# Kernel tuning notes

Measured on AMD Instinct MI355X. Metric: run time of the kernel, lower is better.

## Reference

```python
import jax, jax.numpy as jnp
import numpy as np
from jax import lax

GROUPS = 32
EPS = 1e-5
COMMON_STRIDE = 4


def conv3x3(x, w):
    # x: [B,C,H,W], w: [O,I,3,3], stride 1, padding 1 ('SAME'), no bias
    return lax.conv_general_dilated(x, w, (1, 1), 'SAME',
                                    dimension_numbers=('NCHW', 'OIHW', 'NCHW'))


def group_norm(x, scale, bias):
    b, c, h, w = x.shape
    xg = x.reshape(b, GROUPS, c // GROUPS, h, w)
    mean = xg.mean(axis=(2, 3, 4), keepdims=True)
    var = xg.var(axis=(2, 3, 4), keepdims=True)
    xg = (xg - mean) * lax.rsqrt(var + EPS)
    x = xg.reshape(b, c, h, w)
    return x * scale[None, :, None, None] + bias[None, :, None, None]


def head(x, w, s, bta):
    return jax.nn.relu(group_norm(conv3x3(x, w), s, bta))


def setup_inputs() -> dict:
    key = jax.random.key(0)
    ks = jax.random.split(key, 4)
    B, Cin, H, W = 2, 256, 64, 64
    Cd, K = 128, 19
    fan3 = Cin * 9
    return {
        'x': jax.random.normal(ks[0], (B, Cin, H, W), jnp.float32),
        'w_pam': jax.random.normal(ks[1], (Cd, Cin, 3, 3), jnp.float32) * np.sqrt(2.0 / fan3),
        'gn_pam_scale': jnp.ones((Cd,), jnp.float32),
        'gn_pam_bias': jnp.zeros((Cd,), jnp.float32),
        'w_cam': jax.random.normal(ks[2], (Cd, Cin, 3, 3), jnp.float32) * np.sqrt(2.0 / fan3),
        'gn_cam_scale': jnp.ones((Cd,), jnp.float32),
        'gn_cam_bias': jnp.zeros((Cd,), jnp.float32),
        'w_pred': jax.random.normal(ks[3], (K, Cd, 1, 1), jnp.float32) * np.sqrt(2.0 / Cd),
        'b_pred': jnp.zeros((K,), jnp.float32),
    }


def reference(x, w_pam, gn_pam_scale, gn_pam_bias, w_cam, gn_cam_scale, gn_cam_bias,
              w_pred, b_pred):
    pam = head(x, w_pam, gn_pam_scale, gn_pam_bias)   # [B,C,H,W]
    cam = head(x, w_cam, gn_cam_scale, gn_cam_bias)   # [B,C,H,W]
    b, c, h, w = pam.shape
    n = h * w

    # --- PAM: spatial self-attention, unscaled QK^T softmax V (Q=K=V=pam) ---
    Bm = pam.reshape(b, c, n)                                   # [B,C,N]
    pam_w = jax.nn.softmax(jnp.einsum('bci,bcj->bij', Bm, Bm), axis=-1)  # [B,N,N]
    weighted_pam = jnp.einsum('bij,bcj->bci', pam_w, Bm).reshape(b, c, h, w)
    sum_pam = pam + weighted_pam

    # --- CAM: channel self-attention over [C,C] gram matrix ---
    Am = cam.reshape(b, c, n)                                   # [B,C,N]
    cam_w = jax.nn.softmax(jnp.einsum('bcn,bdn->bcd', Am, Am), axis=-1)  # [B,C,C]
    weighted_cam = jnp.einsum('bcd,bdn->bcn', cam_w, Am).reshape(b, c, h, w)
    sum_cam = cam + weighted_cam

    # --- predictor (1x1 conv with bias) + bilinear upsample x common_stride ---
    fused = sum_pam + sum_cam
    logits = jnp.einsum('bchw,kc->bkhw', fused, w_pred[:, :, 0, 0]) + b_pred[None, :, None, None]
    out = jax.image.resize(logits, (b, logits.shape[1], h * COMMON_STRIDE, w * COMMON_STRIDE),
                           method='bilinear')  # half-pixel centers == align_corners=False
    return out
```

## Files before the change

kernel.cpp:

```cpp
#include <hip/hip_runtime.h>

#define BB 2
#define CIN 256
#define HH 64
#define WW 64
#define NPIX 4096
#define CD 128
#define CO2 256
#define KOUT 19
#define EPSV 1e-5f
#define SPAD 4356
#define KW9 2304

typedef __attribute__((ext_vector_type(8))) short bf16x8;
typedef __attribute__((ext_vector_type(4))) float f32x4;

__device__ inline unsigned short f2bf(float f) {
  unsigned u = __float_as_uint(f);
  u += 0x7fffu + ((u >> 16) & 1u);
  return (unsigned short)(u >> 16);
}
__device__ inline float bf2f(unsigned short h) {
  return __uint_as_float((unsigned)h << 16);
}
__device__ inline void f2bf_pair(float f, unsigned short& hi, unsigned short& lo) {
  hi = f2bf(f);
  const float fhi = __uint_as_float((unsigned)hi << 16);
  lo = f2bf(f - fhi);
}

__global__ __launch_bounds__(256) void zfill_kernel(uint4* __restrict__ p)
{
  const int i = blockIdx.x * 256 + threadIdx.x;
  if (i < 557568) p[i] = make_uint4(0, 0, 0, 0);
}

__global__ __launch_bounds__(256) void xpose_kernel(
    const float* __restrict__ x, unsigned short* __restrict__ xThi,
    unsigned short* __restrict__ xTlo)
{
  const int y = blockIdx.x;
  const int cig = blockIdx.y;
  const int b = blockIdx.z;
  __shared__ float Tl[32][65];
  const int t = threadIdx.x;
  {
    const int cl = t >> 3, pg = t & 7;
    const float* src = x + ((size_t)(b * CIN + cig * 32 + cl)) * NPIX + y * 64 + pg * 8;
    const float4 v0 = *reinterpret_cast<const float4*>(src);
    const float4 v1 = *reinterpret_cast<const float4*>(src + 4);
    Tl[cl][pg * 8 + 0] = v0.x; Tl[cl][pg * 8 + 1] = v0.y;
    Tl[cl][pg * 8 + 2] = v0.z; Tl[cl][pg * 8 + 3] = v0.w;
    Tl[cl][pg * 8 + 4] = v1.x; Tl[cl][pg * 8 + 5] = v1.y;
    Tl[cl][pg * 8 + 6] = v1.z; Tl[cl][pg * 8 + 7] = v1.w;
  }
  __syncthreads();
  {
    const int sl = t >> 2, cg = t & 3;
    unsigned short hh[8], ll[8];
    #pragma unroll
    for (int i = 0; i < 8; ++i) f2bf_pair(Tl[cg * 8 + i][sl], hh[i], ll[i]);
    uint4 ph, pl;
    ph.x = (unsigned)hh[0] | ((unsigned)hh[1] << 16);
    ph.y = (unsigned)hh[2] | ((unsigned)hh[3] << 16);
    ph.z = (unsigned)hh[4] | ((unsigned)hh[5] << 16);
    ph.w = (unsigned)hh[6] | ((unsigned)hh[7] << 16);
    pl.x = (unsigned)ll[0] | ((unsigned)ll[1] << 16);
    pl.y = (unsigned)ll[2] | ((unsigned)ll[3] << 16);
    pl.z = (unsigned)ll[4] | ((unsigned)ll[5] << 16);
    pl.w = (unsigned)ll[6] | ((unsigned)ll[7] << 16);
    const size_t o = ((size_t)b * SPAD + (y + 1) * 66 + 1 + sl) * 256 + cig * 32 + cg * 8;
    *reinterpret_cast<uint4*>(&xThi[o]) = ph;
    *reinterpret_cast<uint4*>(&xTlo[o]) = pl;
  }
}

__global__ __launch_bounds__(256) void wbconv_kernel(
    const float* __restrict__ w_pam, const float* __restrict__ w_cam,
    unsigned short* __restrict__ wbhi, unsigned short* __restrict__ wblo)
{
  const int co = blockIdx.x;
  const float* wsrc = (co < CD) ? (w_pam + (size_t)co * KW9)
                                : (w_cam + (size_t)(co - CD) * KW9);
  const int t = threadIdx.x;
  #pragma unroll
  for (int i = 0; i < 9; ++i) {
    const int idx = i * 256 + t;
    const int q = idx >> 8, ci = idx & 255;
    unsigned short h, l;
    f2bf_pair(wsrc[ci * 9 + q], h, l);
    const size_t dest = ((((size_t)(co >> 4) * 9 + q) * 8 + (ci >> 5)) * 4
                        + ((ci >> 3) & 3)) * 128 + (co & 15) * 8 + (ci & 7);
    wbhi[dest] = h;
    wblo[dest] = l;
  }
}

__global__ __launch_bounds__(256) void conv_mfma_kernel(
    const unsigned short* __restrict__ xThi, const unsigned short* __restrict__ xTlo,
    const unsigned short* __restrict__ wbhi, const unsigned short* __restrict__ wblo,
    float* __restrict__ out)
{
  const int pxt = blockIdx.x;
  const int cot = blockIdx.y;
  const int b = blockIdx.z;
  const int tid = threadIdx.x;
  const int w = tid >> 6;
  const int lane = tid & 63;
  const int m = lane & 15, g = lane >> 4;
  const int p0 = pxt * 64;
  const int y = p0 >> 6;
  const int sbase = (y + 1) * 66 + 1;

  __shared__ float Obuf[4][64][68];

  const size_t xb = (size_t)b * SPAD * 256;

  f32x4 acc[4][4];
  #pragma unroll
  for (int mt = 0; mt < 4; ++mt)
    #pragma unroll
    for (int jg = 0; jg < 4; ++jg)
      #pragma unroll
      for (int r = 0; r < 4; ++r) acc[mt][jg][r] = 0.f;

  for (int q = 0; q < 9; ++q) {
    const int dq = (q / 3 - 1) * 66 + (q % 3 - 1);
    const unsigned short* xh0 = xThi + xb + (size_t)(sbase + m + dq) * 256;
    const unsigned short* xl0 = xTlo + xb + (size_t)(sbase + m + dq) * 256;
    #pragma unroll
    for (int kk2 = 0; kk2 < 2; ++kk2) {
      const int kkc = w * 2 + kk2;
      const int ko = kkc * 32 + g * 8;
      bf16x8 bh[4], bl[4];
      #pragma unroll
      for (int jg = 0; jg < 4; ++jg) {
        bh[jg] = *reinterpret_cast<const bf16x8*>(&xh0[(size_t)(jg * 16) * 256 + ko]);
        bl[jg] = *reinterpret_cast<const bf16x8*>(&xl0[(size_t)(jg * 16) * 256 + ko]);
      }
      #pragma unroll
      for (int mt = 0; mt < 4; ++mt) {
        const size_t wbase = ((((size_t)(cot * 4 + mt) * 9 + q) * 8 + kkc) * 4 + g) * 128
                             + m * 8;
        const bf16x8 ah = *reinterpret_cast<const bf16x8*>(&wbhi[wbase]);
        const bf16x8 al = *reinterpret_cast<const bf16x8*>(&wblo[wbase]);
        #pragma unroll
        for (int jg = 0; jg < 4; ++jg) {
          acc[mt][jg] = __builtin_amdgcn_mfma_f32_16x16x32_bf16(ah, bh[jg], acc[mt][jg], 0, 0, 0);
          acc[mt][jg] = __builtin_amdgcn_mfma_f32_16x16x32_bf16(ah, bl[jg], acc[mt][jg], 0, 0, 0);
          acc[mt][jg] = __builtin_amdgcn_mfma_f32_16x16x32_bf16(al, bh[jg], acc[mt][jg], 0, 0, 0);
        }
      }
    }
  }

  #pragma unroll
  for (int mt = 0; mt < 4; ++mt)
    #pragma unroll
    for (int jg = 0; jg < 4; ++jg)
      #pragma unroll
      for (int r = 0; r < 4; ++r)
        Obuf[w][mt * 16 + g * 4 + r][jg * 16 + m] = acc[mt][jg][r];
  __syncthreads();

  const int co_l = tid >> 2;
  const int pxq = (tid & 3) * 16;
  float* op = out + ((size_t)b * CO2 + cot * 64 + co_l) * NPIX + p0 + pxq;
  #pragma unroll
  for (int i = 0; i < 4; ++i) {
    float4 s;
    s.x = Obuf[0][co_l][pxq + i * 4 + 0] + Obuf[1][co_l][pxq + i * 4 + 0]
        + Obuf[2][co_l][pxq + i * 4 + 0] + Obuf[3][co_l][pxq + i * 4 + 0];
    s.y = Obuf[0][co_l][pxq + i * 4 + 1] + Obuf[1][co_l][pxq + i * 4 + 1]
        + Obuf[2][co_l][pxq + i * 4 + 1] + Obuf[3][co_l][pxq + i * 4 + 1];
    s.z = Obuf[0][co_l][pxq + i * 4 + 2] + Obuf[1][co_l][pxq + i * 4 + 2]
        + Obuf[2][co_l][pxq + i * 4 + 2] + Obuf[3][co_l][pxq + i * 4 + 2];
    s.w = Obuf[0][co_l][pxq + i * 4 + 3] + Obuf[1][co_l][pxq + i * 4 + 3]
        + Obuf[2][co_l][pxq + i * 4 + 3] + Obuf[3][co_l][pxq + i * 4 + 3];
    *reinterpret_cast<float4*>(&op[i * 4]) = s;
  }
}

__global__ __launch_bounds__(256) void gn_stats_kernel(
    const float* __restrict__ conv, float* __restrict__ meanb, float* __restrict__ rstdb)
{
  const int g = blockIdx.x;
  const float* base = conv + (size_t)g * (4 * NPIX);
  float s = 0.f, ss = 0.f;
  const float4* b4 = reinterpret_cast<const float4*>(base);
  for (int i = threadIdx.x; i < 4096; i += 256) {
    float4 v = b4[i];
    s += v.x + v.y + v.z + v.w;
    ss += v.x * v.x + v.y * v.y + v.z * v.z + v.w * v.w;
  }
  #pragma unroll
  for (int off = 32; off > 0; off >>= 1) {
    s += __shfl_down(s, off);
    ss += __shfl_down(ss, off);
  }
  __shared__ float rs[4], rss[4];
  const int lane = threadIdx.x & 63, wv = threadIdx.x >> 6;
  if (lane == 0) { rs[wv] = s; rss[wv] = ss; }
  __syncthreads();
  if (threadIdx.x == 0) {
    const float S = rs[0] + rs[1] + rs[2] + rs[3];
    const float SS = rss[0] + rss[1] + rss[2] + rss[3];
    const float inv = 1.f / 16384.f;
    const float m = S * inv;
    const float var = SS * inv - m * m;
    meanb[g] = m;
    rstdb[g] = rsqrtf(var + EPSV);
  }
}

__global__ __launch_bounds__(256) void gn_apply_kernel(
    float* __restrict__ conv, const float* __restrict__ meanb, const float* __restrict__ rstdb,
    const float* __restrict__ sc_pam, const float* __restrict__ bi_pam,
    const float* __restrict__ sc_cam, const float* __restrict__ bi_cam)
{
  const int idx = blockIdx.x * 256 + threadIdx.x;
  const int call = (idx >> 12) & 255;
  const int g = idx >> 14;
  const int head = call >> 7;
  const int c = call & 127;
  const float sc = head ? sc_cam[c] : sc_pam[c];
  const float bi = head ? bi_cam[c] : bi_pam[c];
  const float v = conv[idx];
  const float r = (v - meanb[g]) * rstdb[g] * sc + bi;
  conv[idx] = fmaxf(r, 0.f);
}

__global__ __launch_bounds__(256) void pack_kv_kernel(
    const float* __restrict__ conv, unsigned short* __restrict__ Kf2,
    unsigned short* __restrict__ Vf2)
{
  const int px0 = blockIdx.x * 64;
  const int c0  = blockIdx.y * 32;
  const int b   = blockIdx.z;
  __shared__ unsigned short Tl[32][76];
  const int t = threadIdx.x;
  {
    const int cl = t >> 3, pg = t & 7;
    const float* src = conv + ((size_t)b * CO2 + c0 + cl) * NPIX + px0 + pg * 8;
    const float4 v0 = *reinterpret_cast<const float4*>(src);
    const float4 v1 = *reinterpret_cast<const float4*>(src + 4);
    Tl[cl][pg * 8 + 0] = f2bf(v0.x); Tl[cl][pg * 8 + 1] = f2bf(v0.y);
    Tl[cl][pg * 8 + 2] = f2bf(v0.z); Tl[cl][pg * 8 + 3] = f2bf(v0.w);
    Tl[cl][pg * 8 + 4] = f2bf(v1.x); Tl[cl][pg * 8 + 5] = f2bf(v1.y);
    Tl[cl][pg * 8 + 6] = f2bf(v1.z); Tl[cl][pg * 8 + 7] = f2bf(v1.w);
  }
  __syncthreads();
  unsigned short* Kb = Kf2 + (size_t)b * 524288;
  unsigned short* Vb = Vf2 + (size_t)b * 524288;
  {
    const int jblk_l = t >> 6, rem = t & 63;
    const int gk = rem >> 4, mk = rem & 15;
    const int jblk = (px0 >> 4) + jblk_l;
    const int kk = c0 >> 5;
    unsigned short h[8];
    #pragma unroll
    for (int e = 0; e < 8; ++e) h[e] = Tl[gk * 8 + e][jblk_l * 16 + mk];
    uint4 packed;
    packed.x = (unsigned)h[0] | ((unsigned)h[1] << 16);
    packed.y = (unsigned)h[2] | ((unsigned)h[3] << 16);
    packed.z = (unsigned)h[4] | ((unsigned)h[5] << 16);
    packed.w = (unsigned)h[6] | ((unsigned)h[7] << 16);
    *reinterpret_cast<uint4*>(&Kb[(size_t)(jblk * 16 + kk * 4 + gk) * 128 + mk * 8]) = packed;
  }
  {
    const int ct_l = t >> 7, kt = (t >> 6) & 1, gv = (t >> 4) & 3, mv = t & 15;
    const int ct = (c0 >> 4) + ct_l;
    const int jc = px0 >> 6;
    unsigned short h[8];
    #pragma unroll
    for (int e = 0; e < 8; ++e) h[e] = Tl[ct_l * 16 + mv][kt * 32 + gv * 8 + e];
    uint4 packed;
    packed.x = (unsigned)h[0] | ((unsigned)h[1] << 16);
    packed.y = (unsigned)h[2] | ((unsigned)h[3] << 16);
    packed.z = (unsigned)h[4] | ((unsigned)h[5] << 16);
    packed.w = (unsigned)h[6] | ((unsigned)h[7] << 16);
    *reinterpret_cast<uint4*>(
        &Vb[(size_t)(((ct * 64 + jc) * 2 + kt) * 4 + gv) * 128 + mv * 8]) = packed;
  }
}

__global__ __launch_bounds__(512) void pam_mfma_kernel(
    const unsigned short* __restrict__ Kf2, const unsigned short* __restrict__ Vf2,
    unsigned short* __restrict__ Opart, float* __restrict__ mpart,
    float* __restrict__ lpart)
{
  const int tile = blockIdx.x;
  const int b = blockIdx.y;
  const int kg = blockIdx.z;
  const int q0 = tile * 32;
  const int tid = threadIdx.x;
  const int w = tid >> 6;
  const int lane = tid & 63;
  const int m = lane & 15, g = lane >> 4;

  __shared__ __align__(16) unsigned short Sl[8][32 * 72];
  __shared__ unsigned short Obuf[4][32][130];
  __shared__ float mlm[8][32], mll[8][32], mst[32], ltt[32];

  const unsigned short* Kb = Kf2 + (size_t)b * 524288;
  const unsigned short* Vb = Vf2 + (size_t)b * 524288;

  bf16x8 qf[2][4];
  #pragma unroll
  for (int s = 0; s < 2; ++s)
    #pragma unroll
    for (int kk = 0; kk < 4; ++kk)
      qf[s][kk] = *reinterpret_cast<const bf16x8*>(
          &Kb[(size_t)(((q0 >> 4) + s) * 16 + kk * 4 + g) * 128 + m * 8]);

  f32x4 oacc[2][8];
  #pragma unroll
  for (int s = 0; s < 2; ++s)
    #pragma unroll
    for (int ct = 0; ct < 8; ++ct)
      #pragma unroll
      for (int r = 0; r < 4; ++r) oacc[s][ct][r] = 0.f;

  float mrow[2][4], lrow[2][4];
  #pragma unroll
  for (int s = 0; s < 2; ++s)
    #pragma unroll
    for (int r = 0; r < 4; ++r) { mrow[s][r] = -1e30f; lrow[s][r] = 0.f; }

  for (int t = kg * 32 + w * 4; t < kg * 32 + w * 4 + 4; ++t) {
    f32x4 sacc[2][4];
    #pragma unroll
    for (int s = 0; s < 2; ++s)
      #pragma unroll
      for (int jt = 0; jt < 4; ++jt)
        #pragma unroll
        for (int r = 0; r < 4; ++r) sacc[s][jt][r] = 0.f;
    #pragma unroll
    for (int jt = 0; jt < 4; ++jt) {
      #pragma unroll
      for (int kk = 0; kk < 4; ++kk) {
        const bf16x8 kf = *reinterpret_cast<const bf16x8*>(
            &Kb[(size_t)((t * 4 + jt) * 16 + kk * 4 + g) * 128 + m * 8]);
        sacc[0][jt] = __builtin_amdgcn_mfma_f32_16x16x32_bf16(qf[0][kk], kf, sacc[0][jt], 0, 0, 0);
        sacc[1][jt] = __builtin_amdgcn_mfma_f32_16x16x32_bf16(qf[1][kk], kf, sacc[1][jt], 0, 0, 0);
      }
    }
    float facq[2];
    #pragma unroll
    for (int s = 0; s < 2; ++s) {
      float fac[4];
      #pragma unroll
      for (int r = 0; r < 4; ++r) {
        float v = fmaxf(fmaxf(sacc[s][0][r], sacc[s][1][r]), fmaxf(sacc[s][2][r], sacc[s][3][r]));
        v = fmaxf(v, __shfl_xor(v, 1));
        v = fmaxf(v, __shfl_xor(v, 2));
        v = fmaxf(v, __shfl_xor(v, 4));
        v = fmaxf(v, __shfl_xor(v, 8));
        const float mn = fmaxf(mrow[s][r], v);
        fac[r] = __expf(fmaxf(mrow[s][r] - mn, -80.f));
        mrow[s][r] = mn;
      }
      #pragma unroll
      for (int r = 0; r < 4; ++r) {
        float ls = 0.f;
        #pragma unroll
        for (int jt = 0; jt < 4; ++jt) {
          const float e = __expf(sacc[s][jt][r] - mrow[s][r]);
          ls += e;
          Sl[w][(s * 16 + g * 4 + r) * 72 + jt * 16 + m] = f2bf(e);
        }
        ls += __shfl_xor(ls, 1);
        ls += __shfl_xor(ls, 2);
        ls += __shfl_xor(ls, 4);
        ls += __shfl_xor(ls, 8);
        lrow[s][r] = lrow[s][r] * fac[r] + ls;
      }
      const int sel = m & 3;
      const float fsel = (sel == 0) ? fac[0] : (sel == 1) ? fac[1] : (sel == 2) ? fac[2] : fac[3];
      facq[s] = __shfl(fsel, ((m >> 2) << 4) | sel);
    }
    #pragma unroll
    for (int s = 0; s < 2; ++s)
      #pragma unroll
      for (int ct = 0; ct < 8; ++ct)
        #pragma unroll
        for (int r = 0; r < 4; ++r) oacc[s][ct][r] *= facq[s];
    bf16x8 pf[2][2];
    #pragma unroll
    for (int s = 0; s < 2; ++s)
      #pragma unroll
      for (int kt = 0; kt < 2; ++kt)
        pf[s][kt] = *reinterpret_cast<const bf16x8*>(&Sl[w][(s * 16 + m) * 72 + kt * 32 + g * 8]);
    #pragma unroll
    for (int ct = 0; ct < 8; ++ct) {
      #pragma unroll
      for (int kt = 0; kt < 2; ++kt) {
        const bf16x8 vf = *reinterpret_cast<const bf16x8*>(
            &Vb[(size_t)(((ct * 64 + t) * 2 + kt) * 4 + g) * 128 + m * 8]);
        oacc[0][ct] = __builtin_amdgcn_mfma_f32_16x16x32_bf16(vf, pf[0][kt], oacc[0][ct], 0, 0, 0);
        oacc[1][ct] = __builtin_amdgcn_mfma_f32_16x16x32_bf16(vf, pf[1][kt], oacc[1][ct], 0, 0, 0);
      }
    }
  }

  float mq[2], lq[2];
  #pragma unroll
  for (int s = 0; s < 2; ++s) {
    const int sel = m & 3;
    const float msel_ = (sel == 0) ? mrow[s][0] : (sel == 1) ? mrow[s][1]
                       : (sel == 2) ? mrow[s][2] : mrow[s][3];
    mq[s] = __shfl(msel_, ((m >> 2) << 4) | sel);
    const float lsel_ = (sel == 0) ? lrow[s][0] : (sel == 1) ? lrow[s][1]
                       : (sel == 2) ? lrow[s][2] : lrow[s][3];
    lq[s] = __shfl(lsel_, ((m >> 2) << 4) | sel);
  }
  if (g == 0) {
    #pragma unroll
    for (int s = 0; s < 2; ++s) { mlm[w][s * 16 + m] = mq[s]; mll[w][s * 16 + m] = lq[s]; }
  }
  __syncthreads();
  float rsw[2];
  #pragma unroll
  for (int s = 0; s < 2; ++s) {
    const int row = s * 16 + m;
    float ms = mlm[0][row];
    #pragma unroll
    for (int sw = 1; sw < 8; ++sw) ms = fmaxf(ms, mlm[sw][row]);
    rsw[s] = __expf(fmaxf(mq[s] - ms, -80.f));
  }
  if (w < 4) {
    #pragma unroll
    for (int s = 0; s < 2; ++s)
      #pragma unroll
      for (int ct = 0; ct < 8; ++ct)
        #pragma unroll
        for (int r = 0; r < 4; ++r)
          Obuf[w][s * 16 + m][ct * 16 + g * 4 + r] = f2bf(oacc[s][ct][r] * rsw[s]);
  }
  if (w == 0 && g == 0) {
    #pragma unroll
    for (int s = 0; s < 2; ++s) {
      const int row = s * 16 + m;
      float ms = mlm[0][row];
      #pragma unroll
      for (int sw = 1; sw < 8; ++sw) ms = fmaxf(ms, mlm[sw][row]);
      float lt = 0.f;
      #pragma unroll
      for (int sw = 0; sw < 8; ++sw)
        lt += mll[sw][row] * __expf(fmaxf(mlm[sw][row] - ms, -80.f));
      mst[row] = ms;
      ltt[row] = lt;
    }
  }
  __syncthreads();
  if (w >= 4) {
    #pragma unroll
    for (int s = 0; s < 2; ++s)
      #pragma unroll
      for (int ct = 0; ct < 8; ++ct)
        #pragma unroll
        for (int r = 0; r < 4; ++r) {
          unsigned short* pp = &Obuf[w - 4][s * 16 + m][ct * 16 + g * 4 + r];
          *pp = f2bf(bf2f(*pp) + oacc[s][ct][r] * rsw[s]);
        }
  }
  __syncthreads();
  const size_t pbase = ((size_t)(kg * BB + b) * 128 + tile) * 32;
  unsigned short* Op = Opart + pbase * 128;
  const int c = tid >> 2;
  const int qh = (tid & 3) * 8;
  #pragma unroll
  for (int qq = 0; qq < 8; ++qq) {
    const int row = qh + qq;
    float o = 0.f;
    #pragma unroll
    for (int sw = 0; sw < 4; ++sw) o += bf2f(Obuf[sw][row][c]);
    Op[(size_t)row * 128 + c] = f2bf(o);
  }
  if (tid < 32) {
    mpart[pbase + tid] = mst[tid];
    lpart[pbase + tid] = ltt[tid];
  }
}

__global__ __launch_bounds__(256) void pam_merge_kernel(
    const float* __restrict__ conv, const unsigned short* __restrict__ Opart,
    const float* __restrict__ mpart, const float* __restrict__ lpart,
    float* __restrict__ spam)
{
  const int tile = blockIdx.x;
  const int b = blockIdx.y;
  const int tid = threadIdx.x;
  const int c = tid & 127;
  const int rg = tid >> 7;
  const size_t i0 = ((size_t)(0 * BB + b) * 128 + tile) * 32;
  const size_t i1 = ((size_t)(1 * BB + b) * 128 + tile) * 32;
  #pragma unroll
  for (int rr = 0; rr < 16; ++rr) {
    const int row = rg * 16 + rr;
    const float m0 = mpart[i0 + row], m1 = mpart[i1 + row];
    const float ms = fmaxf(m0, m1);
    const float w0 = __expf(fmaxf(m0 - ms, -80.f));
    const float w1 = __expf(fmaxf(m1 - ms, -80.f));
    const float l = lpart[i0 + row] * w0 + lpart[i1 + row] * w1;
    const float o = bf2f(Opart[(i0 + row) * 128 + c]) * w0
                  + bf2f(Opart[(i1 + row) * 128 + c]) * w1;
    const int q = tile * 32 + row;
    spam[((size_t)b * CD + c) * NPIX + q] =
        conv[((size_t)b * CO2 + c) * NPIX + q] + o / l;
  }
}

__global__ __launch_bounds__(256) void cam_gram_kernel(
    const float* __restrict__ conv, float* __restrict__ gpart)
{
  const int slice = blockIdx.x;
  const int b = blockIdx.y;
  const float* Am = conv + ((size_t)b * CO2 + CD) * NPIX;
  __shared__ float As[128][65];
  const int tid = threadIdx.x;
  const int cgrp = tid >> 4, dgrp = tid & 15;
  float acc[8][8];
  #pragma unroll
  for (int i = 0; i < 8; ++i)
    #pragma unroll
    for (int j = 0; j < 8; ++j) acc[i][j] = 0.f;
  const int nn = tid & 63, c0 = tid >> 6;
  for (int sub = 0; sub < 2; ++sub) {
    const int n0 = slice * 128 + sub * 64;
    __syncthreads();
    #pragma unroll
    for (int k = 0; k < 32; ++k)
      As[c0 + 4 * k][nn] = Am[(size_t)(c0 + 4 * k) * NPIX + n0 + nn];
    __syncthreads();
    #pragma unroll 4
    for (int n = 0; n < 64; ++n) {
      float av[8], bv[8];
      #pragma unroll
      for (int i = 0; i < 8; ++i) av[i] = As[8 * cgrp + i][n];
      #pragma unroll
      for (int j = 0; j < 8; ++j) bv[j] = As[8 * dgrp + j][n];
      #pragma unroll
      for (int i = 0; i < 8; ++i)
        #pragma unroll
        for (int j = 0; j < 8; ++j)
          acc[i][j] += av[i] * bv[j];
    }
  }
  float* gp = gpart + (((size_t)slice * BB + b) * CD + 8 * cgrp) * CD + 8 * dgrp;
  #pragma unroll
  for (int i = 0; i < 8; ++i)
    #pragma unroll
    for (int j = 0; j < 8; ++j)
      gp[i * CD + j] = acc[i][j];
}

__global__ __launch_bounds__(128) void cam_softmax_kernel(
    const float* __restrict__ gpart, float* __restrict__ camw)
{
  const int bc = blockIdx.x;
  const int b = bc >> 7, c = bc & 127;
  const int d = threadIdx.x;
  float g = 0.f;
  for (int s = 0; s < 32; ++s)
    g += gpart[(((size_t)s * BB + b) * CD + c) * CD + d];
  float m = g;
  #pragma unroll
  for (int off = 32; off > 0; off >>= 1) m = fmaxf(m, __shfl_xor(m, off));
  __shared__ float sm[2], ssum[2];
  const int lane = d & 63, wv = d >> 6;
  if (lane == 0) sm[wv] = m;
  __syncthreads();
  m = fmaxf(sm[0], sm[1]);
  const float e = __expf(g - m);
  float s = e;
  #pragma unroll
  for (int off = 32; off > 0; off >>= 1) s += __shfl_xor(s, off);
  if (lane == 0) ssum[wv] = s;
  __syncthreads();
  camw[(size_t)bc * CD + d] = e / (ssum[0] + ssum[1]);
}

__global__ __launch_bounds__(256) void cam_apply_kernel(
    const float* __restrict__ conv, const float* __restrict__ camw, float* __restrict__ scam)
{
  const int b = blockIdx.z;
  const int c0 = blockIdx.y * 4;
  const int n = blockIdx.x * 1024 + threadIdx.x;
  const float* Am = conv + ((size_t)b * CO2 + CD) * NPIX;
  const float* Wr = camw + ((size_t)b * CD + c0) * CD;
  float acc[4][4];
  #pragma unroll
  for (int i = 0; i < 4; ++i)
    #pragma unroll
    for (int k = 0; k < 4; ++k) acc[i][k] = 0.f;
  for (int d = 0; d < CD; ++d) {
    const float w0 = Wr[d], w1 = Wr[CD + d], w2 = Wr[2 * CD + d], w3 = Wr[3 * CD + d];
    #pragma unroll
    for (int k = 0; k < 4; ++k) {
      const float a = Am[(size_t)d * NPIX + n + k * 256];
      acc[0][k] += w0 * a; acc[1][k] += w1 * a;
      acc[2][k] += w2 * a; acc[3][k] += w3 * a;
    }
  }
  #pragma unroll
  for (int i = 0; i < 4; ++i)
    #pragma unroll
    for (int k = 0; k < 4; ++k)
      scam[((size_t)b * CD + c0 + i) * NPIX + n + k * 256] =
          Am[(size_t)(c0 + i) * NPIX + n + k * 256] + acc[i][k];
}

__global__ __launch_bounds__(256) void pred_part_kernel(
    const float* __restrict__ spam, const float* __restrict__ scam,
    const float* __restrict__ wpred, float* __restrict__ psum)
{
  const int p = blockIdx.x * 256 + threadIdx.x;
  const int slice = blockIdx.y;
  const int b = blockIdx.z;
  float acc[KOUT];
  #pragma unroll
  for (int k = 0; k < KOUT; ++k) acc[k] = 0.f;
  const float* sp = spam + (size_t)b * CD * NPIX + p;
  const float* sc = scam + (size_t)b * CD * NPIX + p;
  #pragma unroll
  for (int ci = 0; ci < 16; ++ci) {
    const int c = slice * 16 + ci;
    const float f = sp[(size_t)c * NPIX] + sc[(size_t)c * NPIX];
    #pragma unroll
    for (int k = 0; k < KOUT; ++k)
      acc[k] += f * wpred[k * CD + c];
  }
  #pragma unroll
  for (int k = 0; k < KOUT; ++k)
    psum[(((size_t)slice * BB + b) * KOUT + k) * NPIX + p] = acc[k];
}

__global__ __launch_bounds__(256) void pred_reduce_kernel(
    const float* __restrict__ psum, const float* __restrict__ bpred,
    float* __restrict__ logit)
{
  const int p = blockIdx.x * 256 + threadIdx.x;
  const int b = blockIdx.y;
  #pragma unroll
  for (int k = 0; k < KOUT; ++k) {
    float s = bpred[k];
    #pragma unroll
    for (int sl = 0; sl < 8; ++sl)
      s += psum[(((size_t)sl * BB + b) * KOUT + k) * NPIX + p];
    logit[((size_t)b * KOUT + k) * NPIX + p] = s;
  }
}

__global__ __launch_bounds__(256) void upsample_kernel(
    const float* __restrict__ logit, float* __restrict__ out)
{
  const int idx = blockIdx.x * 256 + threadIdx.x;
  if (idx >= BB * KOUT * 256 * 256) return;
  const int ox = idx & 255;
  const int oy = (idx >> 8) & 255;
  const int plane = idx >> 16;
  const float* src = logit + (size_t)plane * NPIX;
  const float sy = (oy + 0.5f) * 0.25f - 0.5f;
  const float sx = (ox + 0.5f) * 0.25f - 0.5f;
  const float fyf = floorf(sy), fxf = floorf(sx);
  const float wy = sy - fyf, wx = sx - fxf;
  const int y0 = (int)fyf, x0 = (int)fxf;
  const int y0c = y0 < 0 ? 0 : y0;
  const int y1c = (y0 + 1 > 63) ? 63 : y0 + 1;
  const int x0c = x0 < 0 ? 0 : x0;
  const int x1c = (x0 + 1 > 63) ? 63 : x0 + 1;
  const float v00 = src[y0c * 64 + x0c], v01 = src[y0c * 64 + x1c];
  const float v10 = src[y1c * 64 + x0c], v11 = src[y1c * 64 + x1c];
  const float top = v00 + (v01 - v00) * wx;
  const float bot = v10 + (v11 - v10) * wx;
  out[idx] = top + (bot - top) * wy;
}

extern "C" void kernel_launch(void* const* d_in, const int* in_sizes, int n_in,
                              void* d_out, int out_size, void* d_ws, size_t ws_size,
                              hipStream_t stream) {
  (void)in_sizes; (void)n_in; (void)out_size; (void)ws_size;
  const float* x      = (const float*)d_in[0];
  const float* w_pam  = (const float*)d_in[1];
  const float* s_pam  = (const float*)d_in[2];
  const float* b_pam  = (const float*)d_in[3];
  const float* w_cam  = (const float*)d_in[4];
  const float* s_cam  = (const float*)d_in[5];
  const float* b_cam  = (const float*)d_in[6];
  const float* w_pred = (const float*)d_in[7];
  const float* b_pred = (const float*)d_in[8];
  float* out_f = (float*)d_out;
  float* ws0 = (float*)d_ws;

  float* conv  = ws0;
  unsigned short* xThi = (unsigned short*)(ws0 + 2097152);
  unsigned short* xTlo = xThi + (size_t)BB * SPAD * 256;
  unsigned short* wbhi = (unsigned short*)(ws0 + 4327424);
  unsigned short* wblo = wbhi + (size_t)CO2 * KW9;
  float* gpart = ws0 + 3145728;
  unsigned short* Opart = (unsigned short*)(ws0 + 3145728);
  float* mpart = ws0 + 4194304;
  float* lpart = ws0 + 4227072;
  float* psum  = ws0 + 3145728;
  float* camw  = ws0 + 4950016;
  float* meanb = ws0 + 4982784;
  float* rstdb = ws0 + 4982912;
  float* logit = ws0 + 4983040;

  unsigned short* Kf2 = xThi;
  unsigned short* Vf2 = Kf2 + 1048576;

  float* spam = out_f;
  float* scam = out_f + 1048576;

  zfill_kernel<<<2178, 256, 0, stream>>>((uint4*)xThi);
  xpose_kernel<<<dim3(64, 8, 2), 256, 0, stream>>>(x, xThi, xTlo);
  wbconv_kernel<<<256, 256, 0, stream>>>(w_pam, w_cam, wbhi, wblo);
  conv_mfma_kernel<<<dim3(64, 4, 2), 256, 0, stream>>>(xThi, xTlo, wbhi, wblo, conv);
  gn_stats_kernel<<<128, 256, 0, stream>>>(conv, meanb, rstdb);
  gn_apply_kernel<<<8192, 256, 0, stream>>>(conv, meanb, rstdb, s_pam, b_pam, s_cam, b_cam);
  pack_kv_kernel<<<dim3(64, 4, 2), 256, 0, stream>>>(conv, Kf2, Vf2);
  cam_gram_kernel<<<dim3(32, 2), 256, 0, stream>>>(conv, gpart);
  cam_softmax_kernel<<<256, 128, 0, stream>>>(gpart, camw);
  cam_apply_kernel<<<dim3(4, 32, 2), 256, 0, stream>>>(conv, camw, scam);
  pam_mfma_kernel<<<dim3(128, 2, 2), 512, 0, stream>>>(Kf2, Vf2, Opart, mpart, lpart);
  pam_merge_kernel<<<dim3(128, 2), 256, 0, stream>>>(conv, Opart, mpart, lpart, spam);
  pred_part_kernel<<<dim3(16, 8, 2), 256, 0, stream>>>(spam, scam, w_pred, psum);
  pred_reduce_kernel<<<dim3(16, 2), 256, 0, stream>>>(psum, b_pred, logit);
  upsample_kernel<<<9728, 256, 0, stream>>>(logit, out_f);
}
```

Measured before the change: 250.6 us.

## Fuse GroupNorm apply into KV packing, zero only halo, split conv output tiles

Merges the GroupNorm apply+ReLU pass into the K/V bf16 packing kernel, so the conv output is read once for normalization and packing instead of twice. K/V packing is now limited to the PAM channels. The full padded-buffer zero fill is replaced by a kernel that zeroes only the halo rows and columns. The conv kernel now computes 32 output channels per block instead of 64, doubling the grid for more parallelism and halving accumulator registers. This costs twice the input-tile reads per output and adds an extra LDS reduction step.

```diff
diff --git a/kernel.cpp b/kernel.cpp
--- a/kernel.cpp
+++ b/kernel.cpp
@@ -29,10 +29,18 @@
   lo = f2bf(f - fhi);
 }
 
-__global__ __launch_bounds__(256) void zfill_kernel(uint4* __restrict__ p)
-{
-  const int i = blockIdx.x * 256 + threadIdx.x;
-  if (i < 557568) p[i] = make_uint4(0, 0, 0, 0);
+__global__ __launch_bounds__(64) void zhalo_kernel(
+    unsigned short* __restrict__ xThi, unsigned short* __restrict__ xTlo)
+{
+  const int p = blockIdx.x;
+  const int b = blockIdx.y;
+  int s;
+  if (p < 66) s = p;
+  else if (p < 132) s = 65 * 66 + (p - 66);
+  else { const int q = p - 132; s = (1 + (q >> 1)) * 66 + (q & 1) * 65; }
+  const size_t o = ((size_t)b * SPAD + s) * 256 + threadIdx.x * 4;
+  *reinterpret_cast<uint2*>(&xThi[o]) = make_uint2(0, 0);
+  *reinterpret_cast<uint2*>(&xTlo[o]) = make_uint2(0, 0);
 }
 
 __global__ __launch_bounds__(256) void xpose_kernel(
@@ -112,13 +120,13 @@
   const int y = p0 >> 6;
   const int sbase = (y + 1) * 66 + 1;
 
-  __shared__ float Obuf[4][64][68];
+  __shared__ float Obuf[2][32][68];
 
   const size_t xb = (size_t)b * SPAD * 256;
 
-  f32x4 acc[4][4];
-  #pragma unroll
-  for (int mt = 0; mt < 4; ++mt)
+  f32x4 acc[2][4];
+  #pragma unroll
+  for (int mt = 0; mt < 2; ++mt)
     #pragma unroll
     for (int jg = 0; jg < 4; ++jg)
       #pragma unroll
@@ -139,8 +147,8 @@
         bl[jg] = *reinterpret_cast<const bf16x8*>(&xl0[(size_t)(jg * 16) * 256 + ko]);
       }
       #pragma unroll
-      for (int mt = 0; mt < 4; ++mt) {
-        const size_t wbase = ((((size_t)(cot * 4 + mt) * 9 + q) * 8 + kkc) * 4 + g) * 128
+      for (int mt = 0; mt < 2; ++mt) {
+        const size_t wbase = ((((size_t)(cot * 2 + mt) * 9 + q) * 8 + kkc) * 4 + g) * 128
                              + m * 8;
         const bf16x8 ah = *reinterpret_cast<const bf16x8*>(&wbhi[wbase]);
         const bf16x8 al = *reinterpret_cast<const bf16x8*>(&wblo[wbase]);
@@ -154,29 +162,37 @@
     }
   }
 
-  #pragma unroll
-  for (int mt = 0; mt < 4; ++mt)
-    #pragma unroll
-    for (int jg = 0; jg < 4; ++jg)
-      #pragma unroll
-      for (int r = 0; r < 4; ++r)
-        Obuf[w][mt * 16 + g * 4 + r][jg * 16 + m] = acc[mt][jg][r];
-  __syncthreads();
-
-  const int co_l = tid >> 2;
-  const int pxq = (tid & 3) * 16;
-  float* op = out + ((size_t)b * CO2 + cot * 64 + co_l) * NPIX + p0 + pxq;
-  #pragma unroll
-  for (int i = 0; i < 4; ++i) {
+  if (w < 2) {
+    #pragma unroll
+    for (int mt = 0; mt < 2; ++mt)
+      #pragma unroll
+      for (int jg = 0; jg < 4; ++jg)
+        #pragma unroll
+        for (int r = 0; r < 4; ++r)
+          Obuf[w][mt * 16 + g * 4 + r][jg * 16 + m] = acc[mt][jg][r];
+  }
+  __syncthreads();
+  if (w >= 2) {
+    #pragma unroll
+    for (int mt = 0; mt < 2; ++mt)
+      #pragma unroll
+      for (int jg = 0; jg < 4; ++jg)
+        #pragma unroll
+        for (int r = 0; r < 4; ++r)
+          Obuf[w - 2][mt * 16 + g * 4 + r][jg * 16 + m] += acc[mt][jg][r];
+  }
+  __syncthreads();
+
+  const int co_l = tid >> 3;
+  const int px8 = (tid & 7) * 8;
+  float* op = out + ((size_t)b * CO2 + cot * 32 + co_l) * NPIX + p0 + px8;
+  #pragma unroll
+  for (int i = 0; i < 2; ++i) {
     float4 s;
-    s.x = Obuf[0][co_l][pxq + i * 4 + 0] + Obuf[1][co_l][pxq + i * 4 + 0]
-        + Obuf[2][co_l][pxq + i * 4 + 0] + Obuf[3][co_l][pxq + i * 4 + 0];
-    s.y = Obuf[0][co_l][pxq + i * 4 + 1] + Obuf[1][co_l][pxq + i * 4 + 1]
-        + Obuf[2][co_l][pxq + i * 4 + 1] + Obuf[3][co_l][pxq + i * 4 + 1];
-    s.z = Obuf[0][co_l][pxq + i * 4 + 2] + Obuf[1][co_l][pxq + i * 4 + 2]
-        + Obuf[2][co_l][pxq + i * 4 + 2] + Obuf[3][co_l][pxq + i * 4 + 2];
-    s.w = Obuf[0][co_l][pxq + i * 4 + 3] + Obuf[1][co_l][pxq + i * 4 + 3]
-        + Obuf[2][co_l][pxq + i * 4 + 3] + Obuf[3][co_l][pxq + i * 4 + 3];
+    s.x = Obuf[0][co_l][px8 + i * 4 + 0] + Obuf[1][co_l][px8 + i * 4 + 0];
+    s.y = Obuf[0][co_l][px8 + i * 4 + 1] + Obuf[1][co_l][px8 + i * 4 + 1];
+    s.z = Obuf[0][co_l][px8 + i * 4 + 2] + Obuf[1][co_l][px8 + i * 4 + 2];
+    s.w = Obuf[0][co_l][px8 + i * 4 + 3] + Obuf[1][co_l][px8 + i * 4 + 3];
     *reinterpret_cast<float4*>(&op[i * 4]) = s;
   }
 }
@@ -213,26 +229,11 @@
   }
 }
 
-__global__ __launch_bounds__(256) void gn_apply_kernel(
+__global__ __launch_bounds__(256) void gn_pack_kernel(
     float* __restrict__ conv, const float* __restrict__ meanb, const float* __restrict__ rstdb,
     const float* __restrict__ sc_pam, const float* __restrict__ bi_pam,
-    const float* __restrict__ sc_cam, const float* __restrict__ bi_cam)
-{
-  const int idx = blockIdx.x * 256 + threadIdx.x;
-  const int call = (idx >> 12) & 255;
-  const int g = idx >> 14;
-  const int head = call >> 7;
-  const int c = call & 127;
-  const float sc = head ? sc_cam[c] : sc_pam[c];
-  const float bi = head ? bi_cam[c] : bi_pam[c];
-  const float v = conv[idx];
-  const float r = (v - meanb[g]) * rstdb[g] * sc + bi;
-  conv[idx] = fmaxf(r, 0.f);
-}
-
-__global__ __launch_bounds__(256) void pack_kv_kernel(
-    const float* __restrict__ conv, unsigned short* __restrict__ Kf2,
-    unsigned short* __restrict__ Vf2)
+    const float* __restrict__ sc_cam, const float* __restrict__ bi_cam,
+    unsigned short* __restrict__ Kf2, unsigned short* __restrict__ Vf2)
 {
   const int px0 = blockIdx.x * 64;
   const int c0  = blockIdx.y * 32;
@@ -241,46 +242,64 @@
   const int t = threadIdx.x;
   {
     const int cl = t >> 3, pg = t & 7;
-    const float* src = conv + ((size_t)b * CO2 + c0 + cl) * NPIX + px0 + pg * 8;
-    const float4 v0 = *reinterpret_cast<const float4*>(src);
-    const float4 v1 = *reinterpret_cast<const float4*>(src + 4);
+    const int c = c0 + cl;
+    const int gi = (b * 256 + c) >> 2;
+    const int head = c >> 7, cc = c & 127;
+    const float mean = meanb[gi], rstd = rstdb[gi];
+    const float sc = head ? sc_cam[cc] : sc_pam[cc];
+    const float bi = head ? bi_cam[cc] : bi_pam[cc];
+    float* src = conv + ((size_t)b * CO2 + c) * NPIX + px0 + pg * 8;
+    float4 v0 = *reinterpret_cast<const float4*>(src);
+    float4 v1 = *reinterpret_cast<const float4*>(src + 4);
+    v0.x = fmaxf((v0.x - mean) * rstd * sc + bi, 0.f);
+    v0.y = fmaxf((v0.y - mean) * rstd * sc + bi, 0.f);
+    v0.z = fmaxf((v0.z - mean) * rstd * sc + bi, 0.f);
+    v0.w = fmaxf((v0.w - mean) * rstd * sc + bi, 0.f);
+    v1.x = fmaxf((v1.x - mean) * rstd * sc + bi, 0.f);
+    v1.y = fmaxf((v1.y - mean) * rstd * sc + bi, 0.f);
+    v1.z = fmaxf((v1.z - mean) * rstd * sc + bi, 0.f);
+    v1.w = fmaxf((v1.w - mean) * rstd * sc + bi, 0.f);
+    *reinterpret_cast<float4*>(src) = v0;
+    *reinterpret_cast<float4*>(src + 4) = v1;
     Tl[cl][pg * 8 + 0] = f2bf(v0.x); Tl[cl][pg * 8 + 1] = f2bf(v0.y);
     Tl[cl][pg * 8 + 2] = f2bf(v0.z); Tl[cl][pg * 8 + 3] = f2bf(v0.w);
     Tl[cl][pg * 8 + 4] = f2bf(v1.x); Tl[cl][pg * 8 + 5] = f2bf(v1.y);
     Tl[cl][pg * 8 + 6] = f2bf(v1.z); Tl[cl][pg * 8 + 7] = f2bf(v1.w);
   }
   __syncthreads();
-  unsigned short* Kb = Kf2 + (size_t)b * 524288;
-  unsigned short* Vb = Vf2 + (size_t)b * 524288;
-  {
-    const int jblk_l = t >> 6, rem = t & 63;
-    const int gk = rem >> 4, mk = rem & 15;
-    const int jblk = (px0 >> 4) + jblk_l;
-    const int kk = c0 >> 5;
-    unsigned short h[8];
-    #pragma unroll
-    for (int e = 0; e < 8; ++e) h[e] = Tl[gk * 8 + e][jblk_l * 16 + mk];
-    uint4 packed;
-    packed.x = (unsigned)h[0] | ((unsigned)h[1] << 16);
-    packed.y = (unsigned)h[2] | ((unsigned)h[3] << 16);
-    packed.z = (unsigned)h[4] | ((unsigned)h[5] << 16);
-    packed.w = (unsigned)h[6] | ((unsigned)h[7] << 16);
-    *reinterpret_cast<uint4*>(&Kb[(size_t)(jblk * 16 + kk * 4 + gk) * 128 + mk * 8]) = packed;
-  }
-  {
-    const int ct_l = t >> 7, kt = (t >> 6) & 1, gv = (t >> 4) & 3, mv = t & 15;
-    const int ct = (c0 >> 4) + ct_l;
-    const int jc = px0 >> 6;
-    unsigned short h[8];
-    #pragma unroll
-    for (int e = 0; e < 8; ++e) h[e] = Tl[ct_l * 16 + mv][kt * 32 + gv * 8 + e];
-    uint4 packed;
-    packed.x = (unsigned)h[0] | ((unsigned)h[1] << 16);
-    packed.y = (unsigned)h[2] | ((unsigned)h[3] << 16);
-    packed.z = (unsigned)h[4] | ((unsigned)h[5] << 16);
-    packed.w = (unsigned)h[6] | ((unsigned)h[7] << 16);
-    *reinterpret_cast<uint4*>(
-        &Vb[(size_t)(((ct * 64 + jc) * 2 + kt) * 4 + gv) * 128 + mv * 8]) = packed;
+  if (c0 < CD) {
+    unsigned short* Kb = Kf2 + (size_t)b * 524288;
+    unsigned short* Vb = Vf2 + (size_t)b * 524288;
+    {
+      const int jblk_l = t >> 6, rem = t & 63;
+      const int gk = rem >> 4, mk = rem & 15;
+      const int jblk = (px0 >> 4) + jblk_l;
+      const int kk = c0 >> 5;
+      unsigned short h[8];
+      #pragma unroll
+      for (int e = 0; e < 8; ++e) h[e] = Tl[gk * 8 + e][jblk_l * 16 + mk];
+      uint4 packed;
+      packed.x = (unsigned)h[0] | ((unsigned)h[1] << 16);
+      packed.y = (unsigned)h[2] | ((unsigned)h[3] << 16);
+      packed.z = (unsigned)h[4] | ((unsigned)h[5] << 16);
+      packed.w = (unsigned)h[6] | ((unsigned)h[7] << 16);
+      *reinterpret_cast<uint4*>(&Kb[(size_t)(jblk * 16 + kk * 4 + gk) * 128 + mk * 8]) = packed;
+    }
+    {
+      const int ct_l = t >> 7, kt = (t >> 6) & 1, gv = (t >> 4) & 3, mv = t & 15;
+      const int ct = (c0 >> 4) + ct_l;
+      const int jc = px0 >> 6;
+      unsigned short h[8];
+      #pragma unroll
+      for (int e = 0; e < 8; ++e) h[e] = Tl[ct_l * 16 + mv][kt * 32 + gv * 8 + e];
+      uint4 packed;
+      packed.x = (unsigned)h[0] | ((unsigned)h[1] << 16);
+      packed.y = (unsigned)h[2] | ((unsigned)h[3] << 16);
+      packed.z = (unsigned)h[4] | ((unsigned)h[5] << 16);
+      packed.w = (unsigned)h[6] | ((unsigned)h[7] << 16);
+      *reinterpret_cast<uint4*>(
+          &Vb[(size_t)(((ct * 64 + jc) * 2 + kt) * 4 + gv) * 128 + mv * 8]) = packed;
+    }
   }
 }
 
@@ -714,13 +733,13 @@
   float* spam = out_f;
   float* scam = out_f + 1048576;
 
-  zfill_kernel<<<2178, 256, 0, stream>>>((uint4*)xThi);
+  zhalo_kernel<<<dim3(260, 2), 64, 0, stream>>>(xThi, xTlo);
   xpose_kernel<<<dim3(64, 8, 2), 256, 0, stream>>>(x, xThi, xTlo);
   wbconv_kernel<<<256, 256, 0, stream>>>(w_pam, w_cam, wbhi, wblo);
-  conv_mfma_kernel<<<dim3(64, 4, 2), 256, 0, stream>>>(xThi, xTlo, wbhi, wblo, conv);
+  conv_mfma_kernel<<<dim3(64, 8, 2), 256, 0, stream>>>(xThi, xTlo, wbhi, wblo, conv);
   gn_stats_kernel<<<128, 256, 0, stream>>>(conv, meanb, rstdb);
-  gn_apply_kernel<<<8192, 256, 0, stream>>>(conv, meanb, rstdb, s_pam, b_pam, s_cam, b_cam);
-  pack_kv_kernel<<<dim3(64, 4, 2), 256, 0, stream>>>(conv, Kf2, Vf2);
+  gn_pack_kernel<<<dim3(64, 8, 2), 256, 0, stream>>>(conv, meanb, rstdb,
+      s_pam, b_pam, s_cam, b_cam, Kf2, Vf2);
   cam_gram_kernel<<<dim3(32, 2), 256, 0, stream>>>(conv, gpart);
   cam_softmax_kernel<<<256, 128, 0, stream>>>(gpart, camw);
   cam_apply_kernel<<<dim3(4, 32, 2), 256, 0, stream>>>(conv, camw, scam);
```

Result: slower. 271.5 us (+8.4%).
